# Kernel optimization log

Measured on AMD Instinct MI355X. Metric: run time of the kernel, lower is better.

The kernel has to match this reference:

```python
import jax, jax.numpy as jnp
import numpy as np

N = 4096      # (num_domains+1) * batch_size
F_IN = 512    # nfeat
HID = 64      # nhid per head
H = 8         # nheads
ALPHA = 0.2   # leaky-relu negative slope
EDGE_P = 0.01 # adjacency density


def setup_inputs() -> dict:
    key = jax.random.key(0)
    k1, k2, k3, k4 = jax.random.split(key, 4)
    x = jax.random.normal(k1, (N, F_IN), dtype=jnp.float32)
    adj = (jax.random.uniform(k2, (N, N)) < EDGE_P).astype(jnp.float32)
    # ensure self-loops so every row has at least one valid edge for softmax
    adj = jnp.maximum(adj, jnp.eye(N, dtype=jnp.float32))
    W = jax.random.normal(k3, (H, F_IN, HID), dtype=jnp.float32) * 0.1
    a = jax.random.normal(k4, (H, 2 * HID), dtype=jnp.float32) * 0.1
    return {"x": x, "adj": adj, "W": W, "a": a}


def reference(x, adj, W, a):
    # Wh: [H, N, HID] -- per-head linear projection
    Wh = jnp.einsum('nf,hfd->hnd', x, W)
    # additive attention logits: e_ij = leakyrelu(a1.Wh_i + a2.Wh_j)
    e_src = jnp.einsum('hnd,hd->hn', Wh, a[:, :HID])   # [H, N]
    e_dst = jnp.einsum('hnd,hd->hn', Wh, a[:, HID:])   # [H, N]
    e = jax.nn.leaky_relu(e_src[:, :, None] + e_dst[:, None, :], ALPHA)  # [H, N, N]
    e = jnp.where(adj[None] > 0, e, jnp.float32(-9e15))
    att = jax.nn.softmax(e, axis=-1)                    # masked softmax over neighbors
    h = jnp.einsum('hnm,hmd->hnd', att, Wh)             # [H, N, HID]
    h = jax.nn.elu(h)                                   # concat=True -> elu per head
    # concat heads: [N, H*HID]
    return jnp.transpose(h, (1, 0, 2)).reshape(N, H * HID)
```

## Files before the change

### kernel.cpp

```cpp
#include <hip/hip_runtime.h>
#include <hip/hip_bf16.h>
#include <math.h>

#define N_NODES 4096
#define F_IN    512
#define HID     64
#define H       8
#define NJ      512
#define ALPHA   0.2f

typedef __bf16 bf16x8 __attribute__((ext_vector_type(8)));
typedef float  f32x4  __attribute__((ext_vector_type(4)));

#define A_CHUNKS (N_NODES * F_IN / 8)
#define B_CHUNKS (NJ * F_IN / 8)

__global__ __launch_bounds__(256) void conv_prep(const float* __restrict__ x,
                                                 const float* __restrict__ W,
                                                 __bf16* __restrict__ AhT,
                                                 __bf16* __restrict__ AlT,
                                                 __bf16* __restrict__ BthT) {
    int id = blockIdx.x * 256 + threadIdx.x;
    if (id < A_CHUNKS) {
        int u  = id & 511;
        int kt = (id >> 9) & 7;
        int bm = id >> 12;
        int r  = u >> 3, c8 = u & 7;
        int col = kt * 64 + ((c8 ^ (r & 7)) << 3);
        const float4* gp = (const float4*)(x + (size_t)(bm * 64 + r) * F_IN + col);
        float4 v0 = gp[0];
        float4 v1 = gp[1];
        float vv[8] = {v0.x, v0.y, v0.z, v0.w, v1.x, v1.y, v1.z, v1.w};
        bf16x8 hv, lv;
        #pragma unroll
        for (int e = 0; e < 8; e++) {
            __bf16 hi = (__bf16)vv[e];
            hv[e] = hi;
            lv[e] = (__bf16)(vv[e] - (float)hi);
        }
        *(bf16x8*)(AhT + (size_t)id * 8) = hv;
        *(bf16x8*)(AlT + (size_t)id * 8) = lv;
    } else {
        int bid = id - A_CHUNKS;
        if (bid < B_CHUNKS) {
            int u  = bid & 511;
            int kt = (bid >> 9) & 7;
            int h  = bid >> 12;
            int r  = u >> 3, c8 = u & 7;
            int kb = kt * 64 + ((c8 ^ (r & 7)) << 3);
            bf16x8 hv;
            #pragma unroll
            for (int e = 0; e < 8; e++) {
                hv[e] = (__bf16)W[((size_t)h * F_IN + kb + e) * HID + r];
            }
            *(bf16x8*)(BthT + (size_t)bid * 8) = hv;
        }
    }
}

__device__ __forceinline__ void async16(void* lds, const void* g) {
    __builtin_amdgcn_global_load_lds(
        (const __attribute__((address_space(1))) unsigned int*)g,
        (__attribute__((address_space(3))) unsigned int*)lds, 16, 0, 0);
}

__global__ __launch_bounds__(256) void wh_gemm(const __bf16* __restrict__ AhT,
                                               const __bf16* __restrict__ AlT,
                                               const __bf16* __restrict__ BthT,
                                               const float* __restrict__ a,
                                               __bf16* __restrict__ Whb,
                                               float* __restrict__ esrc,
                                               float* __restrict__ edst) {
    const int bid = blockIdx.x;
    const int xcd = bid & 7;
    const int s0  = bid >> 3;
    const int bm  = xcd * 8 + (s0 >> 3);
    const int h   = s0 & 7;

    const int tid  = threadIdx.x;
    const int wave = tid >> 6;
    const int lane = tid & 63;
    const int lm = lane & 15;
    const int lq = lane >> 4;

    __shared__ __align__(16) __bf16 smem[2 * 3 * 4096];

    f32x4 acc[4];
    #pragma unroll
    for (int c = 0; c < 4; c++) acc[c] = (f32x4){0.f, 0.f, 0.f, 0.f};

    const __bf16* tA_h = AhT  + (size_t)bm * (8 * 4096);
    const __bf16* tA_l = AlT  + (size_t)bm * (8 * 4096);
    const __bf16* tB   = BthT + (size_t)h  * (8 * 4096);

    const int rowA = wave * 16 + lm;

    auto stage = [&](int buf, int kt2) {
        __bf16* base = smem + buf * 12288;
        const size_t ko = (size_t)kt2 * 4096;
        #pragma unroll
        for (int s = 0; s < 2; s++) {
            int u  = s * 256 + tid;
            int ub = s * 256 + wave * 64;
            async16(base +        ub * 8, tA_h + ko + (size_t)u * 8);
            async16(base + 4096 + ub * 8, tA_l + ko + (size_t)u * 8);
            async16(base + 8192 + ub * 8, tB   + ko + (size_t)u * 8);
        }
    };

    stage(0, 0);

    for (int kt = 0; kt < 8; kt++) {
        const int cur = kt & 1;
        if (kt < 7) {
            stage(1 - cur, kt + 1);
            asm volatile("s_waitcnt vmcnt(6)" ::: "memory");
        } else {
            asm volatile("s_waitcnt vmcnt(0)" ::: "memory");
        }
        __builtin_amdgcn_s_barrier();
        __builtin_amdgcn_sched_barrier(0);

        const __bf16* Ash = smem + cur * 12288;
        const __bf16* Asl = Ash + 4096;
        const __bf16* Bsh = Ash + 8192;

        #pragma unroll
        for (int kh = 0; kh < 2; kh++) {
            const int ce = (((kh << 2) + lq) ^ (lm & 7)) << 3;
            bf16x8 afh = *(const bf16x8*)&Ash[rowA * 64 + ce];
            bf16x8 afl = *(const bf16x8*)&Asl[rowA * 64 + ce];
            bf16x8 bh[4];
            #pragma unroll
            for (int c = 0; c < 4; c++) {
                bh[c] = *(const bf16x8*)&Bsh[(c * 16 + lm) * 64 + ce];
            }
            #pragma unroll
            for (int c = 0; c < 4; c++) {
                acc[c] = __builtin_amdgcn_mfma_f32_16x16x32_bf16(afh, bh[c], acc[c], 0, 0, 0);
                acc[c] = __builtin_amdgcn_mfma_f32_16x16x32_bf16(afl, bh[c], acc[c], 0, 0, 0);
            }
        }
        __builtin_amdgcn_s_barrier();
    }

    float a1c[4], a2c[4];
    #pragma unroll
    for (int c = 0; c < 4; c++) {
        a1c[c] = a[h * 2 * HID + c * 16 + lm];
        a2c[c] = a[h * 2 * HID + HID + c * 16 + lm];
    }

    #pragma unroll
    for (int r = 0; r < 4; r++) {
        int row = bm * 64 + wave * 16 + lq * 4 + r;
        float s1 = 0.f, s2 = 0.f;
        #pragma unroll
        for (int c = 0; c < 4; c++) {
            float v = acc[c][r];
            Whb[(size_t)row * NJ + h * HID + c * 16 + lm] = (__bf16)v;
            s1 += v * a1c[c];
            s2 += v * a2c[c];
        }
        #pragma unroll
        for (int o = 1; o < 16; o <<= 1) {
            s1 += __shfl_xor(s1, o);
            s2 += __shfl_xor(s2, o);
        }
        if (lm == 0) {
            esrc[h * N_NODES + row] = s1;
            edst[h * N_NODES + row] = s2;
        }
    }
}

#define MAXN 128

__global__ __launch_bounds__(256) void gat_attn(const float* __restrict__ adj,
                                                const __bf16* __restrict__ Whb,
                                                const float* __restrict__ esrc,
                                                const float* __restrict__ edst,
                                                float* __restrict__ out) {
    const int i    = blockIdx.x;
    const int tid  = threadIdx.x;
    const int wave = tid >> 6;
    const int lane = tid & 63;
    __shared__ int    nbr[MAXN];
    __shared__ __align__(8)  float2 an[H][MAXN];
    __shared__ float  denom[H];
    __shared__ __align__(16) float4 part[128];
    __shared__ int    cnt;

    if (tid == 0) cnt = 0;
    __syncthreads();

    const unsigned long long lt = (1ull << lane) - 1ull;
    const float4* arow = (const float4*)(adj + (size_t)i * N_NODES);
    float4 q[4];
    #pragma unroll
    for (int cc = 0; cc < 4; cc++) q[cc] = arow[cc * 256 + tid];
    #pragma unroll
    for (int cc = 0; cc < 4; cc++) {
        unsigned long long b0 = __ballot(q[cc].x > 0.f);
        unsigned long long b1 = __ballot(q[cc].y > 0.f);
        unsigned long long b2 = __ballot(q[cc].z > 0.f);
        unsigned long long b3 = __ballot(q[cc].w > 0.f);
        int c0 = __popcll(b0), c1 = __popcll(b1), c2 = __popcll(b2), c3 = __popcll(b3);
        int base = 0;
        if (lane == 0) base = atomicAdd(&cnt, c0 + c1 + c2 + c3);
        base = __shfl(base, 0);
        int col = (cc * 256 + tid) * 4;
        if (q[cc].x > 0.f) nbr[base + __popcll(b0 & lt)] = col;
        base += c0;
        if (q[cc].y > 0.f) nbr[base + __popcll(b1 & lt)] = col + 1;
        base += c1;
        if (q[cc].z > 0.f) nbr[base + __popcll(b2 & lt)] = col + 2;
        base += c2;
        if (q[cc].w > 0.f) nbr[base + __popcll(b3 & lt)] = col + 3;
    }
    __syncthreads();
    const int n = cnt;

    #pragma unroll
    for (int k = 0; k < 2; k++) {
        const int h = wave * 2 + k;
        float es = esrc[h * N_NODES + i];
        float m = -1e30f;
        for (int j = lane; j < n; j += 64) {
            int c = nbr[j];
            float lg = es + edst[h * N_NODES + c];
            lg = lg > 0.f ? lg : ALPHA * lg;
            an[h][j] = make_float2(lg, __int_as_float(c << 10));
            m = fmaxf(m, lg);
        }
        #pragma unroll
        for (int o = 32; o; o >>= 1) m = fmaxf(m, __shfl_xor(m, o));
        float s = 0.f;
        for (int j = lane; j < n; j += 64) {
            float w = __expf(an[h][j].x - m);
            an[h][j].x = w;
            s += w;
        }
        #pragma unroll
        for (int o = 32; o; o >>= 1) s += __shfl_xor(s, o);
        if (lane == 0) denom[h] = s;
    }
    __syncthreads();

    const int qd = tid >> 7;
    const int t  = tid & 127;
    const int h  = t >> 4;
    const char* wp = (const char*)Whb + t * 8;
    float a0 = 0.f, a1 = 0.f, a2 = 0.f, a3 = 0.f;
    #pragma unroll 4
    for (int j = qd; j < n; j += 2) {
        float2 p = an[h][j];
        uint2 u = *(const uint2*)(wp + __float_as_uint(p.y));
        float w = p.x;
        a0 += w * __uint_as_float(u.x << 16);
        a1 += w * __uint_as_float(u.x & 0xffff0000u);
        a2 += w * __uint_as_float(u.y << 16);
        a3 += w * __uint_as_float(u.y & 0xffff0000u);
    }
    if (qd) part[t] = make_float4(a0, a1, a2, a3);
    __syncthreads();
    if (qd == 0) {
        float4 p = part[t];
        a0 += p.x; a1 += p.y; a2 += p.z; a3 += p.w;
        float inv = 1.f / denom[h];
        a0 *= inv; a1 *= inv; a2 *= inv; a3 *= inv;
        a0 = a0 > 0.f ? a0 : expm1f(a0);
        a1 = a1 > 0.f ? a1 : expm1f(a1);
        a2 = a2 > 0.f ? a2 : expm1f(a2);
        a3 = a3 > 0.f ? a3 : expm1f(a3);
        *(float4*)(out + (size_t)i * NJ + t * 4) = make_float4(a0, a1, a2, a3);
    }
}

extern "C" void kernel_launch(void* const* d_in, const int* in_sizes, int n_in,
                              void* d_out, int out_size, void* d_ws, size_t ws_size,
                              hipStream_t stream) {
    const float* x   = (const float*)d_in[0];
    const float* adj = (const float*)d_in[1];
    const float* W   = (const float*)d_in[2];
    const float* a   = (const float*)d_in[3];
    float* out = (float*)d_out;

    float*  esrc = (float*)d_ws;
    float*  edst = esrc + (size_t)H * N_NODES;
    __bf16* Whb  = (__bf16*)(edst + (size_t)H * N_NODES);
    __bf16* AhT  = Whb + (size_t)N_NODES * NJ;
    __bf16* AlT  = AhT + (size_t)N_NODES * F_IN;
    __bf16* BthT = AlT + (size_t)N_NODES * F_IN;

    conv_prep<<<(A_CHUNKS + B_CHUNKS) / 256, 256, 0, stream>>>(x, W, AhT, AlT, BthT);

    wh_gemm<<<512, 256, 0, stream>>>(AhT, AlT, BthT, a, Whb, esrc, edst);

    gat_attn<<<N_NODES, 256, 0, stream>>>(adj, Whb, esrc, edst, out);
}
```

Measured before the change: 130.0 us.

## Move adjacency compaction into the prep kernel, concurrent with bf16 conversion

The per-row adjacency scan and neighbor compaction moves out of the attention kernel and into the first prep kernel. Its extra blocks run alongside the x/W bf16 split conversion, and the compacted lists go to global memory. The attention kernel then only loads a small neighbor list per row instead of streaming a 16 KB adjacency row. This trades a small global write and read of the index lists for overlapping the 64 MB adjacency read with the conversion work, which is latency-bound.

```diff
diff --git a/kernel.cpp b/kernel.cpp
--- a/kernel.cpp
+++ b/kernel.cpp
@@ -8,19 +8,64 @@
 #define H       8
 #define NJ      512
 #define ALPHA   0.2f
+#define MAXN    128
 
 typedef __bf16 bf16x8 __attribute__((ext_vector_type(8)));
 typedef float  f32x4  __attribute__((ext_vector_type(4)));
 
 #define A_CHUNKS (N_NODES * F_IN / 8)
 #define B_CHUNKS (NJ * F_IN / 8)
-
-__global__ __launch_bounds__(256) void conv_prep(const float* __restrict__ x,
-                                                 const float* __restrict__ W,
-                                                 __bf16* __restrict__ AhT,
-                                                 __bf16* __restrict__ AlT,
-                                                 __bf16* __restrict__ BthT) {
-    int id = blockIdx.x * 256 + threadIdx.x;
+#define PREP_BLOCKS ((A_CHUNKS + B_CHUNKS) / 256)
+
+__global__ __launch_bounds__(256) void prep_compact(const float* __restrict__ x,
+                                                    const float* __restrict__ W,
+                                                    const float* __restrict__ adj,
+                                                    __bf16* __restrict__ AhT,
+                                                    __bf16* __restrict__ AlT,
+                                                    __bf16* __restrict__ BthT,
+                                                    int* __restrict__ nbr_g,
+                                                    int* __restrict__ cnt_g) {
+    if (blockIdx.x < N_NODES) {
+        const int i    = blockIdx.x;
+        const int tid  = threadIdx.x;
+        const int lane = tid & 63;
+        __shared__ int nbr[MAXN];
+        __shared__ int cnt;
+        if (tid == 0) cnt = 0;
+        __syncthreads();
+
+        const unsigned long long lt = (1ull << lane) - 1ull;
+        const float4* arow = (const float4*)(adj + (size_t)i * N_NODES);
+        float4 q[4];
+        #pragma unroll
+        for (int cc = 0; cc < 4; cc++) q[cc] = arow[cc * 256 + tid];
+        #pragma unroll
+        for (int cc = 0; cc < 4; cc++) {
+            unsigned long long b0 = __ballot(q[cc].x > 0.f);
+            unsigned long long b1 = __ballot(q[cc].y > 0.f);
+            unsigned long long b2 = __ballot(q[cc].z > 0.f);
+            unsigned long long b3 = __ballot(q[cc].w > 0.f);
+            int c0 = __popcll(b0), c1 = __popcll(b1), c2 = __popcll(b2), c3 = __popcll(b3);
+            int base = 0;
+            if (lane == 0) base = atomicAdd(&cnt, c0 + c1 + c2 + c3);
+            base = __shfl(base, 0);
+            int col = (cc * 256 + tid) * 4;
+            if (q[cc].x > 0.f) nbr[base + __popcll(b0 & lt)] = col;
+            base += c0;
+            if (q[cc].y > 0.f) nbr[base + __popcll(b1 & lt)] = col + 1;
+            base += c1;
+            if (q[cc].z > 0.f) nbr[base + __popcll(b2 & lt)] = col + 2;
+            base += c2;
+            if (q[cc].w > 0.f) nbr[base + __popcll(b3 & lt)] = col + 3;
+        }
+        __syncthreads();
+        const int n = cnt;
+        if (tid < n) nbr_g[i * MAXN + tid] = nbr[tid];
+        if (tid == 0) cnt_g[i] = n;
+        return;
+    }
+
+    int id = (blockIdx.x - N_NODES) * 256 + threadIdx.x;
     if (id < A_CHUNKS) {
         int u  = id & 511;
         int kt = (id >> 9) & 7;
@@ -174,9 +219,8 @@
     }
 }
 
-#define MAXN 128
-
-__global__ __launch_bounds__(256) void gat_attn(const float* __restrict__ adj,
+__global__ __launch_bounds__(256) void gat_attn(const int* __restrict__ nbr_g,
+                                                const int* __restrict__ cnt_g,
                                                 const __bf16* __restrict__ Whb,
                                                 const float* __restrict__ esrc,
                                                 const float* __restrict__ edst,
@@ -189,37 +233,10 @@
     __shared__ __align__(8)  float2 an[H][MAXN];
     __shared__ float  denom[H];
     __shared__ __align__(16) float4 part[128];
-    __shared__ int    cnt;
-
-    if (tid == 0) cnt = 0;
+
+    const int n = cnt_g[i];
+    if (tid < n) nbr[tid] = nbr_g[i * MAXN + tid];
     __syncthreads();
-
-    const unsigned long long lt = (1ull << lane) - 1ull;
-    const float4* arow = (const float4*)(adj + (size_t)i * N_NODES);
-    float4 q[4];
-    #pragma unroll
-    for (int cc = 0; cc < 4; cc++) q[cc] = arow[cc * 256 + tid];
-    #pragma unroll
-    for (int cc = 0; cc < 4; cc++) {
-        unsigned long long b0 = __ballot(q[cc].x > 0.f);
-        unsigned long long b1 = __ballot(q[cc].y > 0.f);
-        unsigned long long b2 = __ballot(q[cc].z > 0.f);
-        unsigned long long b3 = __ballot(q[cc].w > 0.f);
-        int c0 = __popcll(b0), c1 = __popcll(b1), c2 = __popcll(b2), c3 = __popcll(b3);
-        int base = 0;
-        if (lane == 0) base = atomicAdd(&cnt, c0 + c1 + c2 + c3);
-        base = __shfl(base, 0);
-        int col = (cc * 256 + tid) * 4;
-        if (q[cc].x > 0.f) nbr[base + __popcll(b0 & lt)] = col;
-        base += c0;
-        if (q[cc].y > 0.f) nbr[base + __popcll(b1 & lt)] = col + 1;
-        base += c1;
-        if (q[cc].z > 0.f) nbr[base + __popcll(b2 & lt)] = col + 2;
-        base += c2;
-        if (q[cc].w > 0.f) nbr[base + __popcll(b3 & lt)] = col + 3;
-    }
-    __syncthreads();
-    const int n = cnt;
 
     #pragma unroll
     for (int k = 0; k < 2; k++) {
@@ -292,10 +309,13 @@
     __bf16* AhT  = Whb + (size_t)N_NODES * NJ;
     __bf16* AlT  = AhT + (size_t)N_NODES * F_IN;
     __bf16* BthT = AlT + (size_t)N_NODES * F_IN;
-
-    conv_prep<<<(A_CHUNKS + B_CHUNKS) / 256, 256, 0, stream>>>(x, W, AhT, AlT, BthT);
+    int*    nbr_g = (int*)(BthT + (size_t)NJ * F_IN);
+    int*    cnt_g = nbr_g + (size_t)N_NODES * MAXN;
+
+    prep_compact<<<N_NODES + PREP_BLOCKS, 256, 0, stream>>>(x, W, adj, AhT, AlT, BthT,
+                                                            nbr_g, cnt_g);
 
     wh_gemm<<<512, 256, 0, stream>>>(AhT, AlT, BthT, a, Whb, esrc, edst);
 
-    gat_attn<<<N_NODES, 256, 0, stream>>>(adj, Whb, esrc, edst, out);
-}
+    gat_attn<<<N_NODES, 256, 0, stream>>>(nbr_g, cnt_g, Whb, esrc, edst, out);
+}
```

New measurement: 131.4 us. About the same (+1.1%).
